# Optimization experiments

Measured on AMD Instinct MI355X. Metric: run time of the kernel, lower is better.

The kernel has to match this reference:

```python
import jax, jax.numpy as jnp
import numpy as np

N = 8192
E = 131072
NODE_DIM = 128
HIDDEN_DIM = 256


def setup_inputs() -> dict:
    key = jax.random.key(0)
    k1, k2, k3 = jax.random.split(key, 3)
    x = jax.random.normal(k1, (N, NODE_DIM), dtype=jnp.float32)
    edge_index = jax.random.randint(k2, (2, E), 0, N, dtype=jnp.int64)
    # nn.Linear(node_dim, hidden_dim, bias=False): weight [hidden_dim, node_dim]
    W = jax.random.normal(k3, (HIDDEN_DIM, NODE_DIM), dtype=jnp.float32) * (1.0 / np.sqrt(NODE_DIM))
    return {"x": x, "edge_index": edge_index, "W": W}


def reference(x, edge_index, W):
    num_nodes = x.shape[0]
    src, tgt = edge_index[0], edge_index[1]
    # Dense adjacency: A[src, tgt] = 1 (set semantics, duplicates collapse)
    A = jnp.zeros((num_nodes, num_nodes), dtype=x.dtype).at[src, tgt].set(1.0)
    A_tilde = A + jnp.eye(num_nodes, dtype=x.dtype)
    D = A_tilde.sum(axis=1)
    D_inv_sqrt = D ** -0.5
    # D_tilde @ A_tilde @ D_tilde == row/col scaling of A_tilde
    A_hat = D_inv_sqrt[:, None] * A_tilde * D_inv_sqrt[None, :]
    out = A_hat @ x            # [N, node_dim]
    out = out @ W.T            # [N, hidden_dim]
    return out
```

## Files before the change

### kernel.cpp

```cpp
#include <hip/hip_runtime.h>

#define N_NODES 8192
#define NODE_DIM 128
#define HIDDEN_DIM 256
#define CAP 96
#define RPB 16
#define YLD 136

typedef __attribute__((ext_vector_type(8))) short bf16x8;
typedef __attribute__((ext_vector_type(4))) float f32x4;

static __device__ __forceinline__ unsigned short f2bf(float f) {
    unsigned u = __builtin_bit_cast(unsigned, f);
    unsigned r = u + 0x7fffu + ((u >> 16) & 1u);
    return (unsigned short)(r >> 16);
}
static __device__ __forceinline__ float bf2f(unsigned short h) {
    unsigned u = ((unsigned)h) << 16;
    return __builtin_bit_cast(float, u);
}

__global__ void append_kernel(const int* __restrict__ e,
                              unsigned int* __restrict__ deg,
                              int* __restrict__ rowlist,
                              const float* __restrict__ W,
                              unsigned short* __restrict__ wh,
                              unsigned short* __restrict__ wl,
                              int E, int nEdgeBlocks) {
    if ((int)blockIdx.x < nEdgeBlocks) {
        int idx = blockIdx.x * 256 + threadIdx.x;
        if (idx >= E) return;
        int s = e[idx];
        int t = e[E + idx];
        unsigned int p = atomicAdd(&deg[s], 1u);
        if (p < CAP) rowlist[(size_t)s * CAP + p] = t;
    } else {
        int t = (blockIdx.x - nEdgeBlocks) * 256 + threadIdx.x;
        if (t >= HIDDEN_DIM * NODE_DIM / 4) return;
        float4 v = ((const float4*)W)[t];
        ushort4 h, l;
        h.x = f2bf(v.x); l.x = f2bf(v.x - bf2f(h.x));
        h.y = f2bf(v.y); l.y = f2bf(v.y - bf2f(h.y));
        h.z = f2bf(v.z); l.z = f2bf(v.z - bf2f(h.z));
        h.w = f2bf(v.w); l.w = f2bf(v.w - bf2f(h.w));
        ((ushort4*)wh)[t] = h;
        ((ushort4*)wl)[t] = l;
    }
}

__global__ __launch_bounds__(256)
void compact_kernel(int* __restrict__ rowlist, unsigned int* __restrict__ deg) {
    __shared__ int buf[4][64];
    int w    = threadIdx.x >> 6;
    int lane = threadIdx.x & 63;
    int i    = blockIdx.x * 4 + w;
    int n = (int)deg[i];
    if (n > 64) n = 64;
    int t = -1;
    if (lane < n) t = rowlist[(size_t)i * CAP + lane];
    buf[w][lane] = t;
    __syncthreads();
    bool keep = false;
    if (lane < n) {
        keep = true;
        for (int j = 0; j < lane; ++j) {
            if (buf[w][j] == t) { keep = false; break; }
        }
    }
    unsigned long long m = __ballot(keep);
    int pos = __popcll(m & ((1ull << lane) - 1ull));
    if (keep && pos != lane) rowlist[(size_t)i * CAP + pos] = t;
    if (lane == 0) deg[i] = (unsigned int)__popcll(m);
}

__global__ __launch_bounds__(512)
void fused_agg_gemm(const int* __restrict__ rowlist,
                    const unsigned int* __restrict__ deg,
                    const float* __restrict__ x,
                    const unsigned short* __restrict__ Wh,
                    const unsigned short* __restrict__ Wl,
                    float* __restrict__ out) {
    __shared__ int            nrow[RPB];
    __shared__ float          sdi[RPB];
    __shared__ int            cols[RPB][CAP];
    __shared__ float          djs[RPB][CAP];
    __shared__ unsigned short Yh[RPB][YLD];
    __shared__ unsigned short Yl[RPB][YLD];

    int tid = threadIdx.x;
    int m0  = blockIdx.x * RPB;

    if (tid < RPB) {
        unsigned int dg = deg[m0 + tid];
        int n = (int)dg; if (n > CAP) n = CAP;
        nrow[tid] = n;
        sdi[tid]  = rsqrtf((float)dg + 1.0f);
    }
    __syncthreads();

    for (int e = tid; e < RPB * CAP; e += 512) {
        int r = e / CAP, k = e - r * CAP;
        if (k < nrow[r]) {
            int c = rowlist[(size_t)(m0 + r) * CAP + k];
            cols[r][k] = c;
            djs[r][k]  = rsqrtf((float)deg[c] + 1.0f);
        }
    }
    __syncthreads();

    {
        int team = tid >> 5;
        int l4   = tid & 31;
        const float4* x4 = (const float4*)x;
        int   n    = nrow[team];
        float di   = sdi[team];
        float4 self = x4[(size_t)(m0 + team) * 32 + l4];
        float ax = 0.f, ay = 0.f, az = 0.f, aw = 0.f;
        int k = 0;
        for (; k + 2 <= n; k += 2) {
            float  d0 = djs[team][k];
            float  d1 = djs[team][k + 1];
            float4 v0 = x4[(size_t)cols[team][k]     * 32 + l4];
            float4 v1 = x4[(size_t)cols[team][k + 1] * 32 + l4];
            ax += d0 * v0.x + d1 * v1.x;
            ay += d0 * v0.y + d1 * v1.y;
            az += d0 * v0.z + d1 * v1.z;
            aw += d0 * v0.w + d1 * v1.w;
        }
        if (k < n) {
            float  d0 = djs[team][k];
            float4 v0 = x4[(size_t)cols[team][k] * 32 + l4];
            ax += d0 * v0.x; ay += d0 * v0.y; az += d0 * v0.z; aw += d0 * v0.w;
        }
        float vx = di * (di * self.x + ax);
        float vy = di * (di * self.y + ay);
        float vz = di * (di * self.z + az);
        float vw = di * (di * self.w + aw);
        ushort4 h, l;
        h.x = f2bf(vx); l.x = f2bf(vx - bf2f(h.x));
        h.y = f2bf(vy); l.y = f2bf(vy - bf2f(h.y));
        h.z = f2bf(vz); l.z = f2bf(vz - bf2f(h.z));
        h.w = f2bf(vw); l.w = f2bf(vw - bf2f(h.w));
        *(ushort4*)&Yh[team][l4 * 4] = h;
        *(ushort4*)&Yl[team][l4 * 4] = l;
    }
    __syncthreads();

    {
        int wave = tid >> 6;
        int lane = tid & 63;
        int quad = lane >> 4;
        int l16  = lane & 15;

        f32x4 acc[2] = {{0,0,0,0},{0,0,0,0}};
#pragma unroll
        for (int ks = 0; ks < 4; ++ks) {
            bf16x8 ah = *(const bf16x8*)&Yh[l16][ks * 32 + quad * 8];
            bf16x8 al = *(const bf16x8*)&Yl[l16][ks * 32 + quad * 8];
#pragma unroll
            for (int ct = 0; ct < 2; ++ct) {
                int hcol = wave * 32 + ct * 16 + l16;
                bf16x8 bh = *(const bf16x8*)(Wh + (size_t)hcol * NODE_DIM + ks * 32 + quad * 8);
                bf16x8 bl = *(const bf16x8*)(Wl + (size_t)hcol * NODE_DIM + ks * 32 + quad * 8);
                acc[ct] = __builtin_amdgcn_mfma_f32_16x16x32_bf16(ah, bh, acc[ct], 0, 0, 0);
                acc[ct] = __builtin_amdgcn_mfma_f32_16x16x32_bf16(ah, bl, acc[ct], 0, 0, 0);
                acc[ct] = __builtin_amdgcn_mfma_f32_16x16x32_bf16(al, bh, acc[ct], 0, 0, 0);
            }
        }
#pragma unroll
        for (int ct = 0; ct < 2; ++ct) {
#pragma unroll
            for (int r = 0; r < 4; ++r) {
                out[(size_t)(m0 + quad * 4 + r) * HIDDEN_DIM + wave * 32 + ct * 16 + l16] = acc[ct][r];
            }
        }
    }
}

extern "C" void kernel_launch(void* const* d_in, const int* in_sizes, int n_in,
                              void* d_out, int out_size, void* d_ws, size_t ws_size,
                              hipStream_t stream) {
    const float* x = (const float*)d_in[0];
    const int*   e = (const int*)d_in[1];
    const float* W = (const float*)d_in[2];
    float*       out = (float*)d_out;
    int E = in_sizes[1] / 2;

    unsigned int*   deg     = (unsigned int*)d_ws;
    int*            rowlist = (int*)(deg + N_NODES);
    unsigned short* wh      = (unsigned short*)(rowlist + (size_t)N_NODES * CAP);
    unsigned short* wl      = wh + (size_t)HIDDEN_DIM * NODE_DIM;

    hipMemsetAsync(d_ws, 0, (size_t)N_NODES * sizeof(unsigned int), stream);

    int nEdgeBlocks = (E + 255) / 256;
    int nWBlocks    = (HIDDEN_DIM * NODE_DIM / 4 + 255) / 256;
    append_kernel<<<nEdgeBlocks + nWBlocks, 256, 0, stream>>>(e, deg, rowlist,
                                                              W, wh, wl, E, nEdgeBlocks);
    compact_kernel<<<N_NODES / 4, 256, 0, stream>>>(rowlist, deg);
    fused_agg_gemm<<<N_NODES / RPB, 512, 0, stream>>>(rowlist, deg, x, wh, wl, out);
}
```

Before: 90.27 us.

## Merge memset, edge append and dedup into one cooperative kernel with grid syncs

Replaces the memset, append kernel and compact kernel with a single cooperative build kernel of 256x512 threads that zeroes degrees, splits W into bf16 hi/lo, appends edges with atomics, and deduplicates each row, separated by grid-wide syncs. Deduplication now compares via wave shuffles instead of a shared-memory buffer. The aim is to remove launch and memset overhead between the small preprocessing stages. In exchange, grid syncs add barrier cost and only 256 blocks are available for the atomic edge pass.

```diff
diff --git a/kernel.cpp b/kernel.cpp
--- a/kernel.cpp
+++ b/kernel.cpp
@@ -1,4 +1,7 @@
 #include <hip/hip_runtime.h>
+#include <hip/hip_cooperative_groups.h>
+
+namespace cg = cooperative_groups;
 
 #define N_NODES 8192
 #define NODE_DIM 128
@@ -20,57 +23,59 @@
     return __builtin_bit_cast(float, u);
 }
 
-__global__ void append_kernel(const int* __restrict__ e,
-                              unsigned int* __restrict__ deg,
-                              int* __restrict__ rowlist,
-                              const float* __restrict__ W,
-                              unsigned short* __restrict__ wh,
-                              unsigned short* __restrict__ wl,
-                              int E, int nEdgeBlocks) {
-    if ((int)blockIdx.x < nEdgeBlocks) {
-        int idx = blockIdx.x * 256 + threadIdx.x;
-        if (idx >= E) return;
-        int s = e[idx];
-        int t = e[E + idx];
-        unsigned int p = atomicAdd(&deg[s], 1u);
-        if (p < CAP) rowlist[(size_t)s * CAP + p] = t;
-    } else {
-        int t = (blockIdx.x - nEdgeBlocks) * 256 + threadIdx.x;
-        if (t >= HIDDEN_DIM * NODE_DIM / 4) return;
-        float4 v = ((const float4*)W)[t];
+__global__ __launch_bounds__(512)
+void build_kernel(const int* __restrict__ e,
+                  unsigned int* __restrict__ deg,
+                  int* __restrict__ rowlist,
+                  const float* __restrict__ W,
+                  unsigned short* __restrict__ wh,
+                  unsigned short* __restrict__ wl,
+                  int E) {
+    cg::grid_group grid = cg::this_grid();
+    int gtid = (int)(blockIdx.x * 512 + threadIdx.x);
+
+    if (gtid < N_NODES) deg[gtid] = 0u;
+    int wi = gtid - N_NODES;
+    if (wi >= 0 && wi < HIDDEN_DIM * NODE_DIM / 4) {
+        float4 v = ((const float4*)W)[wi];
         ushort4 h, l;
         h.x = f2bf(v.x); l.x = f2bf(v.x - bf2f(h.x));
         h.y = f2bf(v.y); l.y = f2bf(v.y - bf2f(h.y));
         h.z = f2bf(v.z); l.z = f2bf(v.z - bf2f(h.z));
         h.w = f2bf(v.w); l.w = f2bf(v.w - bf2f(h.w));
-        ((ushort4*)wh)[t] = h;
-        ((ushort4*)wl)[t] = l;
-    }
-}
-
-__global__ __launch_bounds__(256)
-void compact_kernel(int* __restrict__ rowlist, unsigned int* __restrict__ deg) {
-    __shared__ int buf[4][64];
-    int w    = threadIdx.x >> 6;
-    int lane = threadIdx.x & 63;
-    int i    = blockIdx.x * 4 + w;
-    int n = (int)deg[i];
-    if (n > 64) n = 64;
-    int t = -1;
-    if (lane < n) t = rowlist[(size_t)i * CAP + lane];
-    buf[w][lane] = t;
-    __syncthreads();
-    bool keep = false;
-    if (lane < n) {
-        keep = true;
-        for (int j = 0; j < lane; ++j) {
-            if (buf[w][j] == t) { keep = false; break; }
-        }
-    }
-    unsigned long long m = __ballot(keep);
-    int pos = __popcll(m & ((1ull << lane) - 1ull));
-    if (keep && pos != lane) rowlist[(size_t)i * CAP + pos] = t;
-    if (lane == 0) deg[i] = (unsigned int)__popcll(m);
+        ((ushort4*)wh)[wi] = h;
+        ((ushort4*)wl)[wi] = l;
+    }
+    grid.sync();
+
+    for (int idx = gtid; idx < E; idx += 256 * 512) {
+        int s = e[idx];
+        int t = e[E + idx];
+        unsigned int p = atomicAdd(&deg[s], 1u);
+        if (p < CAP) rowlist[(size_t)s * CAP + p] = t;
+    }
+    grid.sync();
+
+    {
+        int lane = (int)(threadIdx.x & 63);
+        int wgl  = gtid >> 6;
+#pragma unroll
+        for (int rr = 0; rr < 4; ++rr) {
+            int i = wgl * 4 + rr;
+            int n = (int)deg[i];
+            if (n > 64) n = 64;
+            int t = (lane < n) ? rowlist[(size_t)i * CAP + lane] : -1;
+            bool keep = (lane < n);
+            for (int j = 0; j + 1 < n; ++j) {
+                int tj = __shfl(t, j);
+                if (j < lane && tj == t) keep = false;
+            }
+            unsigned long long m = __ballot(keep);
+            int pos = __popcll(m & ((1ull << lane) - 1ull));
+            if (keep && pos != lane) rowlist[(size_t)i * CAP + pos] = t;
+            if (lane == 0) deg[i] = (unsigned int)__popcll(m);
+        }
+    }
 }
 
 __global__ __launch_bounds__(512)
@@ -191,12 +196,18 @@
     unsigned short* wh      = (unsigned short*)(rowlist + (size_t)N_NODES * CAP);
     unsigned short* wl      = wh + (size_t)HIDDEN_DIM * NODE_DIM;
 
-    hipMemsetAsync(d_ws, 0, (size_t)N_NODES * sizeof(unsigned int), stream);
-
-    int nEdgeBlocks = (E + 255) / 256;
-    int nWBlocks    = (HIDDEN_DIM * NODE_DIM / 4 + 255) / 256;
-    append_kernel<<<nEdgeBlocks + nWBlocks, 256, 0, stream>>>(e, deg, rowlist,
-                                                              W, wh, wl, E, nEdgeBlocks);
-    compact_kernel<<<N_NODES / 4, 256, 0, stream>>>(rowlist, deg);
+    {
+        const int*      e_arg  = e;
+        unsigned int*   d_arg  = deg;
+        int*            r_arg  = rowlist;
+        const float*    W_arg  = W;
+        unsigned short* wh_arg = wh;
+        unsigned short* wl_arg = wl;
+        int             E_arg  = E;
+        void* args[] = {(void*)&e_arg, (void*)&d_arg, (void*)&r_arg,
+                        (void*)&W_arg, (void*)&wh_arg, (void*)&wl_arg, (void*)&E_arg};
+        hipLaunchCooperativeKernel((const void*)build_kernel, dim3(256), dim3(512),
+                                   args, 0, stream);
+    }
     fused_agg_gemm<<<N_NODES / RPB, 512, 0, stream>>>(rowlist, deg, x, wh, wl, out);
 }
```

Result: slower. 160.2 us (+77.4%).
